# Kernel optimization log

Hardware: AMD Instinct MI355X
Metric: run time of the kernel (lower is better)

## Reference

```python
import jax, jax.numpy as jnp
import numpy as np

B, T, TKV, D, H = 4, 2048, 512, 1024, 16
HD = D // H  # 64
HIDDEN = ((int(D * 4 * 2 / 3) + 7) // 8) * 8  # 2736
EPS = 1e-6


def setup_inputs() -> dict:
    key = jax.random.key(0)
    ks = jax.random.split(key, 16)
    x = jax.random.normal(ks[0], (B, T, D), jnp.float32)
    memory = jax.random.normal(ks[1], (B, TKV, D), jnp.float32)
    # RoPE frequencies: (T, HD//2, 2) = (cos, sin)
    inv_freq = 1.0 / (10000.0 ** (jnp.arange(0, HD, 2, dtype=jnp.float32) / HD))
    angles = jnp.arange(T, dtype=jnp.float32)[:, None] * inv_freq[None, :]
    freqs_cis = jnp.stack([jnp.cos(angles), jnp.sin(angles)], axis=-1)
    # causal mask (T, T): 0 on/below diag, -inf above
    causal_mask = jnp.where(jnp.tril(jnp.ones((T, T), bool)), 0.0, -jnp.inf).astype(jnp.float32)
    s = 0.02
    w = lambda k, i, o: jax.random.normal(k, (i, o), jnp.float32) * s  # stored as (in, out)
    return {
        'x': x, 'memory': memory, 'freqs_cis': freqs_cis, 'causal_mask': causal_mask,
        'sa_wq': w(ks[2], D, D), 'sa_wk': w(ks[3], D, D), 'sa_wv': w(ks[4], D, D), 'sa_wo': w(ks[5], D, D),
        'ca_wq': w(ks[6], D, D), 'ca_wk': w(ks[7], D, D), 'ca_wv': w(ks[8], D, D), 'ca_wo': w(ks[9], D, D),
        'w1': w(ks[10], D, HIDDEN), 'w3': w(ks[11], D, HIDDEN), 'w2': w(ks[12], HIDDEN, D),
        'g_sa': jnp.ones((D,), jnp.float32), 'g_ca': jnp.ones((D,), jnp.float32), 'g_ffn': jnp.ones((D,), jnp.float32),
    }


def rmsnorm(x, g):
    return x * jax.lax.rsqrt(jnp.mean(x * x, axis=-1, keepdims=True) + EPS) * g


def apply_rope(t, f):
    # t: (B, H, T, HD); f: (T, HD//2, 2)
    tr = t.reshape(*t.shape[:-1], HD // 2, 2)
    a, b = tr[..., 0], tr[..., 1]
    cos, sin = f[None, None, :, :, 0], f[None, None, :, :, 1]
    out = jnp.stack([a * cos - b * sin, a * sin + b * cos], axis=-1)
    return out.reshape(t.shape)


def heads(x, w):
    # (B, S, D) @ (D, D) -> (B, H, S, HD)
    b, s, _ = x.shape
    return (x @ w).reshape(b, s, H, HD).transpose(0, 2, 1, 3)


def attention(xq, kv, wq, wk, wv, wo, freqs=None, mask=None):
    q, k, v = heads(xq, wq), heads(kv, wk), heads(kv, wv)
    if freqs is not None:
        q, k = apply_rope(q, freqs), apply_rope(k, freqs)
    attn = jnp.einsum('bhqd,bhkd->bhqk', q, k) * (HD ** -0.5)
    if mask is not None:
        attn = attn + mask
    attn = jax.nn.softmax(attn, axis=-1)
    out = jnp.einsum('bhqk,bhkd->bhqd', attn, v)
    out = out.transpose(0, 2, 1, 3).reshape(xq.shape[0], xq.shape[1], D)
    return out @ wo


def reference(x, memory, freqs_cis, causal_mask,
              sa_wq, sa_wk, sa_wv, sa_wo,
              ca_wq, ca_wk, ca_wv, ca_wo,
              w1, w2, w3, g_sa, g_ca, g_ffn):
    x = rmsnorm(x + attention(x, x, sa_wq, sa_wk, sa_wv, sa_wo, freqs=freqs_cis, mask=causal_mask), g_sa)
    x = rmsnorm(x + attention(x, memory, ca_wq, ca_wk, ca_wv, ca_wo), g_ca)
    ffn = (jax.nn.silu(x @ w1) * (x @ w3)) @ w2
    x = rmsnorm(x + ffn, g_ffn)
    return x
```

## Files before the change

kernel.cpp:

```cpp
#include <hip/hip_runtime.h>
#include <hip/hip_bf16.h>

typedef __attribute__((ext_vector_type(8))) short s16x8;
typedef __attribute__((ext_vector_type(4))) float f32x4;
typedef __attribute__((ext_vector_type(16))) float f32x16;
typedef unsigned short u16;
typedef unsigned int u32;
typedef unsigned long long u64;

#define MFMA(a,b,c) __builtin_amdgcn_mfma_f32_16x16x32_bf16(a,b,c,0,0,0)
#define MFMA32(a,b,c) __builtin_amdgcn_mfma_f32_32x32x16_bf16(a,b,c,0,0,0)

constexpr int B_ = 4, T_ = 2048, TKV_ = 512, D_ = 1024, H_ = 16, HD_ = 64;
constexpr int HID_ = 2736, HIDP_ = 2816;

__device__ __forceinline__ float bf2f(u16 x) {
    union { float f; u32 u; } c; c.u = ((u32)x) << 16; return c.f;
}
__device__ __forceinline__ u16 f2bf(float f) {
    union { float f; u32 u; } c; c.f = f;
    u32 r = c.u + 0x7fffu + ((c.u >> 16) & 1u);
    return (u16)(r >> 16);
}

__device__ __forceinline__ void gload16(const void* g, void* l) {
    __builtin_amdgcn_global_load_lds(
        (const __attribute__((address_space(1))) u32*)g,
        (__attribute__((address_space(3))) u32*)l, 16, 0, 0);
}

__global__ __launch_bounds__(256) void wt_cast(const float* __restrict__ W, u16* __restrict__ WT,
                                               int K, int N, int Kp, int Np) {
    __shared__ float t[32][33];
    int tid = threadIdx.x;
    int tx = tid & 31, ty = tid >> 5;
    int n0 = blockIdx.x * 32, k0 = blockIdx.y * 32;
#pragma unroll
    for (int i = 0; i < 4; ++i) {
        int kk = k0 + ty + i * 8, nn = n0 + tx;
        t[ty + i * 8][tx] = (kk < K && nn < N) ? W[(size_t)kk * N + nn] : 0.f;
    }
    __syncthreads();
#pragma unroll
    for (int i = 0; i < 4; ++i) {
        int nn = n0 + ty + i * 8, kk = k0 + tx;
        WT[(size_t)nn * Kp + kk] = f2bf(t[tx][ty + i * 8]);
    }
}

__global__ __launch_bounds__(256) void cast_bf16(const float* __restrict__ in, u16* __restrict__ out, int n4) {
    int i = blockIdx.x * 256 + threadIdx.x;
    if (i >= n4) return;
    float4 v = ((const float4*)in)[i];
    u64 pk = (u64)f2bf(v.x) | ((u64)f2bf(v.y) << 16) | ((u64)f2bf(v.z) << 32) | ((u64)f2bf(v.w) << 48);
    ((u64*)out)[i] = pk;
}

__global__ __launch_bounds__(256) void gemm_bf16(const u16* __restrict__ A, const u16* __restrict__ Bt,
                                                 void* __restrict__ C, const u16* __restrict__ mul,
                                                 int M, int N, int K, int mode, int nwg) {
    __shared__ __align__(16) u16 As[2][128 * 64];
    __shared__ __align__(16) u16 Bs[2][128 * 64];
    const int tid = threadIdx.x;
    const int lane = tid & 63, wid = tid >> 6;
    const int wr = wid >> 1, wc = wid & 1;
    const int li = lane & 15, g = lane >> 4;

    int bid = (int)blockIdx.x;
    bid = (bid & 7) * (nwg >> 3) + (bid >> 3);

    const int tn = N >> 7;
    const int m0 = (bid / tn) * 128, n0 = (bid % tn) * 128;

    const int rowst = tid >> 3;
    const int colb = (tid & 7) * 16;
    const char* ga = (const char*)A + ((size_t)(m0 + rowst) * K) * 2 + colb;
    const char* gb = (const char*)Bt + ((size_t)(n0 + rowst) * K) * 2 + colb;
    const size_t rstride = (size_t)32 * K * 2;

    f32x4 acc[4][4] = {};
    const int nt = K >> 6;

#pragma unroll
    for (int i = 0; i < 4; ++i) {
        gload16(ga + i * rstride, (char*)As[0] + i * 4096 + wid * 1024);
        gload16(gb + i * rstride, (char*)Bs[0] + i * 4096 + wid * 1024);
    }
    __syncthreads();

    int cur = 0;
    for (int t = 0; t < nt; ++t) {
        if (t + 1 < nt) {
            const char* gan = ga + (size_t)(t + 1) * 128;
            const char* gbn = gb + (size_t)(t + 1) * 128;
#pragma unroll
            for (int i = 0; i < 4; ++i) {
                gload16(gan + i * rstride, (char*)As[cur ^ 1] + i * 4096 + wid * 1024);
                gload16(gbn + i * rstride, (char*)Bs[cur ^ 1] + i * 4096 + wid * 1024);
            }
        }
#pragma unroll
        for (int kk = 0; kk < 2; ++kk) {
            s16x8 aF[4], bF[4];
#pragma unroll
            for (int m = 0; m < 4; ++m) aF[m] = *(const s16x8*)&As[cur][(wr * 64 + m * 16 + li) * 64 + kk * 32 + g * 8];
#pragma unroll
            for (int n = 0; n < 4; ++n) bF[n] = *(const s16x8*)&Bs[cur][(wc * 64 + n * 16 + li) * 64 + kk * 32 + g * 8];
#pragma unroll
            for (int m = 0; m < 4; ++m)
#pragma unroll
                for (int n = 0; n < 4; ++n)
                    acc[m][n] = MFMA(aF[m], bF[n], acc[m][n]);
        }
        __syncthreads();
        cur ^= 1;
    }

#pragma unroll
    for (int m = 0; m < 4; ++m)
#pragma unroll
        for (int n = 0; n < 4; ++n)
#pragma unroll
            for (int r = 0; r < 4; ++r) {
                size_t row = m0 + wr * 64 + m * 16 + g * 4 + r;
                size_t col = n0 + wc * 64 + n * 16 + li;
                size_t idx = row * N + col;
                float v = acc[m][n][r];
                if (mode == 0) {
                    ((float*)C)[idx] = v;
                } else if (mode == 1) {
                    ((u16*)C)[idx] = f2bf(v);
                } else if (mode == 2) {
                    float sg = 1.f / (1.f + __expf(-v));
                    ((u16*)C)[idx] = f2bf(v * sg);
                } else if (mode == 3) {
                    float h = bf2f(mul[idx]);
                    ((u16*)C)[idx] = f2bf(v * h);
                } else {
                    ((u16*)C)[idx] = f2bf(v * 0.125f);
                }
            }
}

__global__ __launch_bounds__(256) void rope_qk(u16* __restrict__ q, u16* __restrict__ k,
                                               const float* __restrict__ fr) {
    size_t idx = (size_t)blockIdx.x * 256 + threadIdx.x;
    int i = (int)(idx & 31);
    int h = (int)((idx >> 5) & 15);
    size_t bt = idx >> 9;
    int t = (int)(bt & (T_ - 1));
    float2 cs = ((const float2*)fr)[t * 32 + i];
    size_t off = bt * D_ + h * 64 + 2 * i;
    {
        u32* p = (u32*)(q + off);
        u32 w = *p;
        float a = bf2f((u16)(w & 0xffff)), b = bf2f((u16)(w >> 16));
        *p = (u32)f2bf((a * cs.x - b * cs.y) * 0.125f) | ((u32)f2bf((a * cs.y + b * cs.x) * 0.125f) << 16);
    }
    {
        u32* p = (u32*)(k + off);
        u32 w = *p;
        float a = bf2f((u16)(w & 0xffff)), b = bf2f((u16)(w >> 16));
        *p = (u32)f2bf(a * cs.x - b * cs.y) | ((u32)f2bf(a * cs.y + b * cs.x) << 16);
    }
}

__global__ __launch_bounds__(256) void vtrans(const u16* __restrict__ v, u16* __restrict__ vT, int Tk) {
    __shared__ u16 tile[32][34];
    int bh = blockIdx.x;
    int t0 = blockIdx.y * 32, d0 = blockIdx.z * 32;
    int b = bh >> 4, h = bh & 15;
    int tid = threadIdx.x;
    int tx = tid & 31, ty = tid >> 5;
#pragma unroll
    for (int i = 0; i < 4; ++i)
        tile[ty + i * 8][tx] = v[((size_t)b * Tk + t0 + ty + i * 8) * D_ + h * 64 + d0 + tx];
    __syncthreads();
#pragma unroll
    for (int i = 0; i < 4; ++i)
        vT[((size_t)bh * 64 + d0 + ty + i * 8) * Tk + t0 + tx] = tile[tx][ty + i * 8];
}

__device__ __forceinline__ void attn32(const u16* __restrict__ qh, const u16* __restrict__ kh,
                                       const u16* __restrict__ vh, u16* __restrict__ oh,
                                       int q0, int nkb, int Tk, int causal, int lq, int hi) {
    const u16* qb = qh + (size_t)(q0 + lq) * D_;
    s16x8 qf[4];
#pragma unroll
    for (int c = 0; c < 4; ++c) qf[c] = *(const s16x8*)&qb[c * 16 + hi * 8];

    f32x16 o0 = {}, o1 = {};
    float mr = -1e30f, lr = 0.f;

    for (int kb = 0; kb < nkb; ++kb) {
        const int ks = kb * 32;
        f32x16 s = {};
        const u16* kp = kh + (size_t)(ks + lq) * D_ + hi * 8;
#pragma unroll
        for (int c = 0; c < 4; ++c) {
            s16x8 kf = *(const s16x8*)&kp[c * 16];
            s = MFMA32(kf, qf[c], s);
        }
        if (causal && kb == nkb - 1) {
#pragma unroll
            for (int r = 0; r < 16; ++r) {
                int kl = (r & 3) + 8 * (r >> 2) + 4 * hi;
                if (kl > lq) s[r] = -1e30f;
            }
        }
        float bm = fmaxf(fmaxf(fmaxf(s[0], s[1]), fmaxf(s[2], s[3])),
                         fmaxf(fmaxf(s[4], s[5]), fmaxf(s[6], s[7])));
        float bm2 = fmaxf(fmaxf(fmaxf(s[8], s[9]), fmaxf(s[10], s[11])),
                          fmaxf(fmaxf(s[12], s[13]), fmaxf(s[14], s[15])));
        bm = fmaxf(bm, bm2);
        bm = fmaxf(bm, __shfl_xor(bm, 32));
        float mn = fmaxf(mr, bm);
        float sc = __expf(mr - mn);
        mr = mn;
        float p[16];
        float rs = 0.f;
#pragma unroll
        for (int r = 0; r < 16; ++r) { p[r] = __expf(s[r] - mn); rs += p[r]; }
        rs += __shfl_xor(rs, 32);
        lr = lr * sc + rs;
#pragma unroll
        for (int r = 0; r < 16; ++r) { o0[r] *= sc; o1[r] *= sc; }

        u32 pk[8];
#pragma unroll
        for (int i = 0; i < 8; ++i)
            pk[i] = (u32)f2bf(p[2 * i]) | ((u32)f2bf(p[2 * i + 1]) << 16);
        u32 e1 = __shfl_xor(hi ? pk[0] : pk[2], 32);
        u32 e2 = __shfl_xor(hi ? pk[1] : pk[3], 32);
        u32 e3 = __shfl_xor(hi ? pk[4] : pk[6], 32);
        u32 e4 = __shfl_xor(hi ? pk[5] : pk[7], 32);
        union { s16x8 v; u32 w[4]; } pf0, pf1;
        pf0.w[0] = hi ? e1 : pk[0];
        pf0.w[1] = hi ? e2 : pk[1];
        pf0.w[2] = hi ? pk[2] : e1;
        pf0.w[3] = hi ? pk[3] : e2;
        pf1.w[0] = hi ? e3 : pk[4];
        pf1.w[1] = hi ? e4 : pk[5];
        pf1.w[2] = hi ? pk[6] : e3;
        pf1.w[3] = hi ? pk[7] : e4;

        const u16* v0 = vh + (size_t)lq * Tk + ks + hi * 8;
        const u16* v1 = vh + (size_t)(32 + lq) * Tk + ks + hi * 8;
        o0 = MFMA32(*(const s16x8*)&v0[0],  pf0.v, o0);
        o0 = MFMA32(*(const s16x8*)&v0[16], pf1.v, o0);
        o1 = MFMA32(*(const s16x8*)&v1[0],  pf0.v, o1);
        o1 = MFMA32(*(const s16x8*)&v1[16], pf1.v, o1);
    }

    float inv = 1.f / lr;
    u16* ob = oh + (size_t)(q0 + lq) * D_;
#pragma unroll
    for (int r = 0; r < 16; ++r) {
        int hd = (r & 3) + 8 * (r >> 2) + 4 * hi;
        ob[hd] = f2bf(o0[r] * inv);
        ob[hd + 32] = f2bf(o1[r] * inv);
    }
}

__global__ __launch_bounds__(256) void attn_causal32(const u16* __restrict__ q, const u16* __restrict__ k,
                                                     const u16* __restrict__ vT, u16* __restrict__ o,
                                                     int Tq, int Tk) {
    const int lane = threadIdx.x & 63, wid = threadIdx.x >> 6;
    const int lq = lane & 31, hi = lane >> 5;
    const int ntile = Tq / 32;
    const int ppb = (ntile / 2) / 4;
    const int bh = blockIdx.x / ppb;
    const int p = (blockIdx.x % ppb) * 4 + wid;
    const int b = bh >> 4, h = bh & 15;

    const u16* qh = q + ((size_t)b * Tq) * D_ + h * 64;
    const u16* kh = k + ((size_t)b * Tk) * D_ + h * 64;
    const u16* vh = vT + ((size_t)bh * 64) * Tk;
    u16* oh = o + ((size_t)b * Tq) * D_ + h * 64;

    const int tA = p, tB = ntile - 1 - p;
    attn32(qh, kh, vh, oh, tA * 32, tA + 1, Tk, 1, lq, hi);
    attn32(qh, kh, vh, oh, tB * 32, tB + 1, Tk, 1, lq, hi);
}

__global__ __launch_bounds__(256) void attn_plain32(const u16* __restrict__ q, const u16* __restrict__ k,
                                                    const u16* __restrict__ vT, u16* __restrict__ o,
                                                    int Tq, int Tk) {
    const int lane = threadIdx.x & 63, wid = threadIdx.x >> 6;
    const int lq = lane & 31, hi = lane >> 5;
    const int tpb = (Tq / 32) / 4;
    const int bh = blockIdx.x / tpb;
    const int qt = (blockIdx.x % tpb) * 4 + wid;
    const int b = bh >> 4, h = bh & 15;

    const u16* qh = q + ((size_t)b * Tq) * D_ + h * 64;
    const u16* kh = k + ((size_t)b * Tk) * D_ + h * 64;
    const u16* vh = vT + ((size_t)bh * 64) * Tk;
    u16* oh = o + ((size_t)b * Tq) * D_ + h * 64;

    attn32(qh, kh, vh, oh, qt * 32, Tk / 32, Tk, 0, lq, hi);
}

__global__ __launch_bounds__(256) void addnorm(const float* __restrict__ xa, const float* __restrict__ xb,
                                               const float* __restrict__ gg, float* __restrict__ fo,
                                               u16* __restrict__ bo) {
    int row = blockIdx.x, tid = threadIdx.x;
    float4 a = ((const float4*)(xa + (size_t)row * D_))[tid];
    float4 b = ((const float4*)(xb + (size_t)row * D_))[tid];
    float vx = a.x + b.x, vy = a.y + b.y, vz = a.z + b.z, vw = a.w + b.w;
    float ss = vx * vx + vy * vy + vz * vz + vw * vw;
    ss += __shfl_xor(ss, 1);
    ss += __shfl_xor(ss, 2);
    ss += __shfl_xor(ss, 4);
    ss += __shfl_xor(ss, 8);
    ss += __shfl_xor(ss, 16);
    ss += __shfl_xor(ss, 32);
    __shared__ float red[4];
    int lane = tid & 63, wid = tid >> 6;
    if (lane == 0) red[wid] = ss;
    __syncthreads();
    float tot = red[0] + red[1] + red[2] + red[3];
    float s = rsqrtf(tot * (1.0f / D_) + 1e-6f);
    float4 gv = ((const float4*)gg)[tid];
    float yx = vx * s * gv.x, yy = vy * s * gv.y, yz = vz * s * gv.z, yw = vw * s * gv.w;
    if (fo) {
        float4 o4; o4.x = yx; o4.y = yy; o4.z = yz; o4.w = yw;
        ((float4*)(fo + (size_t)row * D_))[tid] = o4;
    }
    if (bo) {
        u64 pk = (u64)f2bf(yx) | ((u64)f2bf(yy) << 16) | ((u64)f2bf(yz) << 32) | ((u64)f2bf(yw) << 48);
        ((u64*)(bo + (size_t)row * D_))[tid] = pk;
    }
}

extern "C" void kernel_launch(void* const* d_in, const int* in_sizes, int n_in,
                              void* d_out, int out_size, void* d_ws, size_t ws_size,
                              hipStream_t stream) {
    const float* x    = (const float*)d_in[0];
    const float* mem  = (const float*)d_in[1];
    const float* fr   = (const float*)d_in[2];
    const float* wsaq = (const float*)d_in[4];
    const float* wsak = (const float*)d_in[5];
    const float* wsav = (const float*)d_in[6];
    const float* wsao = (const float*)d_in[7];
    const float* wcaq = (const float*)d_in[8];
    const float* wcak = (const float*)d_in[9];
    const float* wcav = (const float*)d_in[10];
    const float* wcao = (const float*)d_in[11];
    const float* w1   = (const float*)d_in[12];
    const float* w3   = (const float*)d_in[13];
    const float* w2   = (const float*)d_in[14];
    const float* g_sa = (const float*)d_in[15];
    const float* g_ca = (const float*)d_in[16];
    const float* g_ff = (const float*)d_in[17];
    float* outF = (float*)d_out;

    char* p = (char*)d_ws;
    auto alloc = [&](size_t bytes) { char* r = p; p += (bytes + 255) & ~(size_t)255; return r; };
    const size_t DD2 = (size_t)1024 * 1024 * 2;
    u16* saqT = (u16*)alloc(DD2);
    u16* sakT = (u16*)alloc(DD2);
    u16* savT = (u16*)alloc(DD2);
    u16* saoT = (u16*)alloc(DD2);
    u16* caqT = (u16*)alloc(DD2);
    u16* cakT = (u16*)alloc(DD2);
    u16* cavT = (u16*)alloc(DD2);
    u16* caoT = (u16*)alloc(DD2);
    u16* w1T  = (u16*)alloc((size_t)HIDP_ * 1024 * 2);
    u16* w3T  = (u16*)alloc((size_t)HIDP_ * 1024 * 2);
    u16* w2T  = (u16*)alloc((size_t)1024 * HIDP_ * 2);
    u16* Ab   = (u16*)alloc((size_t)8192 * 1024 * 2);
    u16* memb = (u16*)alloc((size_t)2048 * 1024 * 2);
    u16* qb   = (u16*)alloc((size_t)8192 * 1024 * 2);
    u16* kb   = (u16*)alloc((size_t)8192 * 1024 * 2);
    u16* vb   = (u16*)alloc((size_t)8192 * 1024 * 2);
    u16* vtb  = (u16*)alloc((size_t)8192 * 1024 * 2);
    u16* ob   = (u16*)alloc((size_t)8192 * 1024 * 2);
    float* Pf = (float*)alloc((size_t)8192 * 1024 * 4);
    float* Rf = (float*)alloc((size_t)8192 * 1024 * 4);
    u16* Hb   = (u16*)alloc((size_t)8192 * HIDP_ * 2);

    dim3 blk(256);

    wt_cast<<<dim3(32, 32), blk, 0, stream>>>(wsaq, saqT, 1024, 1024, 1024, 1024);
    wt_cast<<<dim3(32, 32), blk, 0, stream>>>(wsak, sakT, 1024, 1024, 1024, 1024);
    wt_cast<<<dim3(32, 32), blk, 0, stream>>>(wsav, savT, 1024, 1024, 1024, 1024);
    wt_cast<<<dim3(32, 32), blk, 0, stream>>>(wsao, saoT, 1024, 1024, 1024, 1024);
    wt_cast<<<dim3(32, 32), blk, 0, stream>>>(wcaq, caqT, 1024, 1024, 1024, 1024);
    wt_cast<<<dim3(32, 32), blk, 0, stream>>>(wcak, cakT, 1024, 1024, 1024, 1024);
    wt_cast<<<dim3(32, 32), blk, 0, stream>>>(wcav, cavT, 1024, 1024, 1024, 1024);
    wt_cast<<<dim3(32, 32), blk, 0, stream>>>(wcao, caoT, 1024, 1024, 1024, 1024);
    wt_cast<<<dim3(88, 32), blk, 0, stream>>>(w1, w1T, 1024, HID_, 1024, HIDP_);
    wt_cast<<<dim3(88, 32), blk, 0, stream>>>(w3, w3T, 1024, HID_, 1024, HIDP_);
    wt_cast<<<dim3(32, 88), blk, 0, stream>>>(w2, w2T, HID_, 1024, HIDP_, 1024);

    cast_bf16<<<8192, blk, 0, stream>>>(x, Ab, 2097152);
    cast_bf16<<<2048, blk, 0, stream>>>(mem, memb, 524288);

    gemm_bf16<<<512, blk, 0, stream>>>(Ab, saqT, qb, nullptr, 8192, 1024, 1024, 1, 512);
    gemm_bf16<<<512, blk, 0, stream>>>(Ab, sakT, kb, nullptr, 8192, 1024, 1024, 1, 512);
    gemm_bf16<<<512, blk, 0, stream>>>(Ab, savT, vb, nullptr, 8192, 1024, 1024, 1, 512);
    rope_qk<<<16384, blk, 0, stream>>>(qb, kb, fr);
    vtrans<<<dim3(64, 64, 2), blk, 0, stream>>>(vb, vtb, 2048);
    attn_causal32<<<512, blk, 0, stream>>>(qb, kb, vtb, ob, 2048, 2048);
    gemm_bf16<<<512, blk, 0, stream>>>(ob, saoT, Pf, nullptr, 8192, 1024, 1024, 0, 512);
    addnorm<<<8192, blk, 0, stream>>>(x, Pf, g_sa, Rf, Ab);

    gemm_bf16<<<512, blk, 0, stream>>>(Ab, caqT, qb, nullptr, 8192, 1024, 1024, 4, 512);
    gemm_bf16<<<128, blk, 0, stream>>>(memb, cakT, kb, nullptr, 2048, 1024, 1024, 1, 128);
    gemm_bf16<<<128, blk, 0, stream>>>(memb, cavT, vb, nullptr, 2048, 1024, 1024, 1, 128);
    vtrans<<<dim3(64, 16, 2), blk, 0, stream>>>(vb, vtb, 512);
    attn_plain32<<<1024, blk, 0, stream>>>(qb, kb, vtb, ob, 2048, 512);
    gemm_bf16<<<512, blk, 0, stream>>>(ob, caoT, Pf, nullptr, 8192, 1024, 1024, 0, 512);
    addnorm<<<8192, blk, 0, stream>>>(Rf, Pf, g_ca, Rf, Ab);

    gemm_bf16<<<64 * 22, blk, 0, stream>>>(Ab, w1T, Hb, nullptr, 8192, HIDP_, 1024, 2, 64 * 22);
    gemm_bf16<<<64 * 22, blk, 0, stream>>>(Ab, w3T, Hb, Hb, 8192, HIDP_, 1024, 3, 64 * 22);
    gemm_bf16<<<512, blk, 0, stream>>>(Hb, w2T, Pf, nullptr, 8192, 1024, HIDP_, 0, 512);
    addnorm<<<8192, blk, 0, stream>>>(Rf, Pf, g_ff, outF, nullptr);
}
```

Before: 945.1 us.

## Add 256x256-tile GEMM kernel and fuse QKV and cross-attention KV projections

```diff
diff --git a/kernel.cpp b/kernel.cpp
--- a/kernel.cpp
+++ b/kernel.cpp
@@ -54,6 +54,22 @@
     float4 v = ((const float4*)in)[i];
     u64 pk = (u64)f2bf(v.x) | ((u64)f2bf(v.y) << 16) | ((u64)f2bf(v.z) << 32) | ((u64)f2bf(v.w) << 48);
     ((u64*)out)[i] = pk;
+}
+
+__device__ __forceinline__ void gemm_store(void* C, const u16* mul, size_t idx, float v, int mode) {
+    if (mode == 0) {
+        ((float*)C)[idx] = v;
+    } else if (mode == 1) {
+        ((u16*)C)[idx] = f2bf(v);
+    } else if (mode == 2) {
+        float sg = 1.f / (1.f + __expf(-v));
+        ((u16*)C)[idx] = f2bf(v * sg);
+    } else if (mode == 3) {
+        float h = bf2f(mul[idx]);
+        ((u16*)C)[idx] = f2bf(v * h);
+    } else {
+        ((u16*)C)[idx] = f2bf(v * 0.125f);
+    }
 }
 
 __global__ __launch_bounds__(256) void gemm_bf16(const u16* __restrict__ A, const u16* __restrict__ Bt,
@@ -124,33 +140,91 @@
             for (int r = 0; r < 4; ++r) {
                 size_t row = m0 + wr * 64 + m * 16 + g * 4 + r;
                 size_t col = n0 + wc * 64 + n * 16 + li;
-                size_t idx = row * N + col;
-                float v = acc[m][n][r];
-                if (mode == 0) {
-                    ((float*)C)[idx] = v;
-                } else if (mode == 1) {
-                    ((u16*)C)[idx] = f2bf(v);
-                } else if (mode == 2) {
-                    float sg = 1.f / (1.f + __expf(-v));
-                    ((u16*)C)[idx] = f2bf(v * sg);
-                } else if (mode == 3) {
-                    float h = bf2f(mul[idx]);
-                    ((u16*)C)[idx] = f2bf(v * h);
-                } else {
-                    ((u16*)C)[idx] = f2bf(v * 0.125f);
-                }
+                gemm_store(C, mul, row * N + col, acc[m][n][r], mode);
+            }
+}
+
+__global__ __launch_bounds__(512) void gemm256(const u16* __restrict__ A, const u16* __restrict__ Bt,
+                                               void* __restrict__ C, const u16* __restrict__ mul,
+                                               int M, int N, int K, int mode, int nwg) {
+    __shared__ __align__(16) u16 As[2][256 * 64];
+    __shared__ __align__(16) u16 Bs[2][256 * 64];
+    const int tid = threadIdx.x;
+    const int lane = tid & 63, wid = tid >> 6;
+    const int wr = wid >> 2, wc = wid & 3;
+    const int li = lane & 15, g = lane >> 4;
+
+    int bid = (int)blockIdx.x;
+    bid = (bid & 7) * (nwg >> 3) + (bid >> 3);
+
+    const int tn = N >> 8;
+    const int m0 = (bid / tn) * 256, n0 = (bid % tn) * 256;
+
+    const int rowst = tid >> 3;
+    const int colb = (tid & 7) * 16;
+    const char* ga = (const char*)A + ((size_t)(m0 + rowst) * K) * 2 + colb;
+    const char* gb = (const char*)Bt + ((size_t)(n0 + rowst) * K) * 2 + colb;
+    const size_t rstride = (size_t)64 * K * 2;
+
+    f32x4 acc[8][4] = {};
+    const int nt = K >> 6;
+
+#pragma unroll
+    for (int i = 0; i < 4; ++i) {
+        gload16(ga + i * rstride, (char*)As[0] + i * 8192 + wid * 1024);
+        gload16(gb + i * rstride, (char*)Bs[0] + i * 8192 + wid * 1024);
+    }
+    __syncthreads();
+
+    int cur = 0;
+    for (int t = 0; t < nt; ++t) {
+        if (t + 1 < nt) {
+            const char* gan = ga + (size_t)(t + 1) * 128;
+            const char* gbn = gb + (size_t)(t + 1) * 128;
+#pragma unroll
+            for (int i = 0; i < 4; ++i) {
+                gload16(gan + i * rstride, (char*)As[cur ^ 1] + i * 8192 + wid * 1024);
+                gload16(gbn + i * rstride, (char*)Bs[cur ^ 1] + i * 8192 + wid * 1024);
+            }
+        }
+#pragma unroll
+        for (int kk = 0; kk < 2; ++kk) {
+            s16x8 bF[4];
+#pragma unroll
+            for (int n = 0; n < 4; ++n) bF[n] = *(const s16x8*)&Bs[cur][(wc * 64 + n * 16 + li) * 64 + kk * 32 + g * 8];
+#pragma unroll
+            for (int m = 0; m < 8; ++m) {
+                s16x8 aF = *(const s16x8*)&As[cur][(wr * 128 + m * 16 + li) * 64 + kk * 32 + g * 8];
+#pragma unroll
+                for (int n = 0; n < 4; ++n)
+                    acc[m][n] = MFMA(aF, bF[n], acc[m][n]);
+            }
+        }
+        __syncthreads();
+        cur ^= 1;
+    }
+
+#pragma unroll
+    for (int m = 0; m < 8; ++m)
+#pragma unroll
+        for (int n = 0; n < 4; ++n)
+#pragma unroll
+            for (int r = 0; r < 4; ++r) {
+                size_t row = m0 + wr * 128 + m * 16 + g * 4 + r;
+                size_t col = n0 + wc * 64 + n * 16 + li;
+                gemm_store(C, mul, row * N + col, acc[m][n][r], mode);
             }
 }
 
 __global__ __launch_bounds__(256) void rope_qk(u16* __restrict__ q, u16* __restrict__ k,
-                                               const float* __restrict__ fr) {
+                                               const float* __restrict__ fr, int S) {
     size_t idx = (size_t)blockIdx.x * 256 + threadIdx.x;
     int i = (int)(idx & 31);
     int h = (int)((idx >> 5) & 15);
     size_t bt = idx >> 9;
     int t = (int)(bt & (T_ - 1));
     float2 cs = ((const float2*)fr)[t * 32 + i];
-    size_t off = bt * D_ + h * 64 + 2 * i;
+    size_t off = bt * (size_t)S + h * 64 + 2 * i;
     {
         u32* p = (u32*)(q + off);
         u32 w = *p;
@@ -165,7 +239,8 @@
     }
 }
 
-__global__ __launch_bounds__(256) void vtrans(const u16* __restrict__ v, u16* __restrict__ vT, int Tk) {
+__global__ __launch_bounds__(256) void vtrans(const u16* __restrict__ v, u16* __restrict__ vT,
+                                              int Tk, int S) {
     __shared__ u16 tile[32][34];
     int bh = blockIdx.x;
     int t0 = blockIdx.y * 32, d0 = blockIdx.z * 32;
@@ -174,7 +249,7 @@
     int tx = tid & 31, ty = tid >> 5;
 #pragma unroll
     for (int i = 0; i < 4; ++i)
-        tile[ty + i * 8][tx] = v[((size_t)b * Tk + t0 + ty + i * 8) * D_ + h * 64 + d0 + tx];
+        tile[ty + i * 8][tx] = v[((size_t)b * Tk + t0 + ty + i * 8) * S + h * 64 + d0 + tx];
     __syncthreads();
 #pragma unroll
     for (int i = 0; i < 4; ++i)
@@ -183,8 +258,9 @@
 
 __device__ __forceinline__ void attn32(const u16* __restrict__ qh, const u16* __restrict__ kh,
                                        const u16* __restrict__ vh, u16* __restrict__ oh,
-                                       int q0, int nkb, int Tk, int causal, int lq, int hi) {
-    const u16* qb = qh + (size_t)(q0 + lq) * D_;
+                                       int q0, int nkb, int Tk, int causal, int lq, int hi,
+                                       int QS, int KS) {
+    const u16* qb = qh + (size_t)(q0 + lq) * QS;
     s16x8 qf[4];
 #pragma unroll
     for (int c = 0; c < 4; ++c) qf[c] = *(const s16x8*)&qb[c * 16 + hi * 8];
@@ -195,7 +271,7 @@
     for (int kb = 0; kb < nkb; ++kb) {
         const int ks = kb * 32;
         f32x16 s = {};
-        const u16* kp = kh + (size_t)(ks + lq) * D_ + hi * 8;
+        const u16* kp = kh + (size_t)(ks + lq) * KS + hi * 8;
 #pragma unroll
         for (int c = 0; c < 4; ++c) {
             s16x8 kf = *(const s16x8*)&kp[c * 16];
@@ -264,7 +340,7 @@
 
 __global__ __launch_bounds__(256) void attn_causal32(const u16* __restrict__ q, const u16* __restrict__ k,
                                                      const u16* __restrict__ vT, u16* __restrict__ o,
-                                                     int Tq, int Tk) {
+                                                     int Tq, int Tk, int QS, int KS) {
     const int lane = threadIdx.x & 63, wid = threadIdx.x >> 6;
     const int lq = lane & 31, hi = lane >> 5;
     const int ntile = Tq / 32;
@@ -273,19 +349,19 @@
     const int p = (blockIdx.x % ppb) * 4 + wid;
     const int b = bh >> 4, h = bh & 15;
 
-    const u16* qh = q + ((size_t)b * Tq) * D_ + h * 64;
-    const u16* kh = k + ((size_t)b * Tk) * D_ + h * 64;
+    const u16* qh = q + ((size_t)b * Tq) * QS + h * 64;
+    const u16* kh = k + ((size_t)b * Tk) * KS + h * 64;
     const u16* vh = vT + ((size_t)bh * 64) * Tk;
     u16* oh = o + ((size_t)b * Tq) * D_ + h * 64;
 
     const int tA = p, tB = ntile - 1 - p;
-    attn32(qh, kh, vh, oh, tA * 32, tA + 1, Tk, 1, lq, hi);
-    attn32(qh, kh, vh, oh, tB * 32, tB + 1, Tk, 1, lq, hi);
+    attn32(qh, kh, vh, oh, tA * 32, tA + 1, Tk, 1, lq, hi, QS, KS);
+    attn32(qh, kh, vh, oh, tB * 32, tB + 1, Tk, 1, lq, hi, QS, KS);
 }
 
 __global__ __launch_bounds__(256) void attn_plain32(const u16* __restrict__ q, const u16* __restrict__ k,
                                                     const u16* __restrict__ vT, u16* __restrict__ o,
-                                                    int Tq, int Tk) {
+                                                    int Tq, int Tk, int QS, int KS) {
     const int lane = threadIdx.x & 63, wid = threadIdx.x >> 6;
     const int lq = lane & 31, hi = lane >> 5;
     const int tpb = (Tq / 32) / 4;
@@ -293,12 +369,12 @@
     const int qt = (blockIdx.x % tpb) * 4 + wid;
     const int b = bh >> 4, h = bh & 15;
 
-    const u16* qh = q + ((size_t)b * Tq) * D_ + h * 64;
-    const u16* kh = k + ((size_t)b * Tk) * D_ + h * 64;
+    const u16* qh = q + ((size_t)b * Tq) * QS + h * 64;
+    const u16* kh = k + ((size_t)b * Tk) * KS + h * 64;
     const u16* vh = vT + ((size_t)bh * 64) * Tk;
     u16* oh = o + ((size_t)b * Tq) * D_ + h * 64;
 
-    attn32(qh, kh, vh, oh, qt * 32, Tk / 32, Tk, 0, lq, hi);
+    attn32(qh, kh, vh, oh, qt * 32, Tk / 32, Tk, 0, lq, hi, QS, KS);
 }
 
 __global__ __launch_bounds__(256) void addnorm(const float* __restrict__ xa, const float* __restrict__ xb,
@@ -358,37 +434,35 @@
     char* p = (char*)d_ws;
     auto alloc = [&](size_t bytes) { char* r = p; p += (bytes + 255) & ~(size_t)255; return r; };
     const size_t DD2 = (size_t)1024 * 1024 * 2;
-    u16* saqT = (u16*)alloc(DD2);
-    u16* sakT = (u16*)alloc(DD2);
-    u16* savT = (u16*)alloc(DD2);
-    u16* saoT = (u16*)alloc(DD2);
-    u16* caqT = (u16*)alloc(DD2);
-    u16* cakT = (u16*)alloc(DD2);
-    u16* cavT = (u16*)alloc(DD2);
-    u16* caoT = (u16*)alloc(DD2);
-    u16* w1T  = (u16*)alloc((size_t)HIDP_ * 1024 * 2);
-    u16* w3T  = (u16*)alloc((size_t)HIDP_ * 1024 * 2);
-    u16* w2T  = (u16*)alloc((size_t)1024 * HIDP_ * 2);
-    u16* Ab   = (u16*)alloc((size_t)8192 * 1024 * 2);
-    u16* memb = (u16*)alloc((size_t)2048 * 1024 * 2);
-    u16* qb   = (u16*)alloc((size_t)8192 * 1024 * 2);
-    u16* kb   = (u16*)alloc((size_t)8192 * 1024 * 2);
-    u16* vb   = (u16*)alloc((size_t)8192 * 1024 * 2);
+    u16* wqkvT = (u16*)alloc(3 * DD2);
+    u16* saoT  = (u16*)alloc(DD2);
+    u16* caqT  = (u16*)alloc(DD2);
+    u16* wkvT  = (u16*)alloc(2 * DD2);
+    u16* caoT  = (u16*)alloc(DD2);
+    u16* w1T   = (u16*)alloc((size_t)HIDP_ * 1024 * 2);
+    u16* w3T   = (u16*)alloc((size_t)HIDP_ * 1024 * 2);
+    u16* w2T   = (u16*)alloc((size_t)1024 * HIDP_ * 2);
+    u16* Ab    = (u16*)alloc((size_t)8192 * 1024 * 2);
+    u16* memb  = (u16*)alloc((size_t)2048 * 1024 * 2);
+    char* qkvRaw = alloc((size_t)8192 * 3072 * 2);
+    u16* qkvb = (u16*)qkvRaw;
+    u16* kvb  = (u16*)qkvRaw;
+    u16* caqb = (u16*)(qkvRaw + (size_t)25165824);
     u16* vtb  = (u16*)alloc((size_t)8192 * 1024 * 2);
     u16* ob   = (u16*)alloc((size_t)8192 * 1024 * 2);
     float* Pf = (float*)alloc((size_t)8192 * 1024 * 4);
     float* Rf = (float*)alloc((size_t)8192 * 1024 * 4);
     u16* Hb   = (u16*)alloc((size_t)8192 * HIDP_ * 2);
 
-    dim3 blk(256);
-
-    wt_cast<<<dim3(32, 32), blk, 0, stream>>>(wsaq, saqT, 1024, 1024, 1024, 1024);
-    wt_cast<<<dim3(32, 32), blk, 0, stream>>>(wsak, sakT, 1024, 1024, 1024, 1024);
-    wt_cast<<<dim3(32, 32), blk, 0, stream>>>(wsav, savT, 1024, 1024, 1024, 1024);
+    dim3 blk(256), blk5(512);
+
+    wt_cast<<<dim3(32, 32), blk, 0, stream>>>(wsaq, wqkvT,               1024, 1024, 1024, 1024);
+    wt_cast<<<dim3(32, 32), blk, 0, stream>>>(wsak, wqkvT + 1024 * 1024, 1024, 1024, 1024, 1024);
+    wt_cast<<<dim3(32, 32), blk, 0, stream>>>(wsav, wqkvT + 2048 * 1024, 1024, 1024, 1024, 1024);
     wt_cast<<<dim3(32, 32), blk, 0, stream>>>(wsao, saoT, 1024, 1024, 1024, 1024);
     wt_cast<<<dim3(32, 32), blk, 0, stream>>>(wcaq, caqT, 1024, 1024, 1024, 1024);
-    wt_cast<<<dim3(32, 32), blk, 0, stream>>>(wcak, cakT, 1024, 1024, 1024, 1024);
-    wt_cast<<<dim3(32, 32), blk, 0, stream>>>(wcav, cavT, 1024, 1024, 1024, 1024);
+    wt_cast<<<dim3(32, 32), blk, 0, stream>>>(wcak, wkvT,               1024, 1024, 1024, 1024);
+    wt_cast<<<dim3(32, 32), blk, 0, stream>>>(wcav, wkvT + 1024 * 1024, 1024, 1024, 1024, 1024);
     wt_cast<<<dim3(32, 32), blk, 0, stream>>>(wcao, caoT, 1024, 1024, 1024, 1024);
     wt_cast<<<dim3(88, 32), blk, 0, stream>>>(w1, w1T, 1024, HID_, 1024, HIDP_);
     wt_cast<<<dim3(88, 32), blk, 0, stream>>>(w3, w3T, 1024, HID_, 1024, HIDP_);
@@ -397,25 +471,22 @@
     cast_bf16<<<8192, blk, 0, stream>>>(x, Ab, 2097152);
     cast_bf16<<<2048, blk, 0, stream>>>(mem, memb, 524288);
 
-    gemm_bf16<<<512, blk, 0, stream>>>(Ab, saqT, qb, nullptr, 8192, 1024, 1024, 1, 512);
-    gemm_bf16<<<512, blk, 0, stream>>>(Ab, sakT, kb, nullptr, 8192, 1024, 1024, 1, 512);
-    gemm_bf16<<<512, blk, 0, stream>>>(Ab, savT, vb, nullptr, 8192, 1024, 1024, 1, 512);
-    rope_qk<<<16384, blk, 0, stream>>>(qb, kb, fr);
-    vtrans<<<dim3(64, 64, 2), blk, 0, stream>>>(vb, vtb, 2048);
-    attn_causal32<<<512, blk, 0, stream>>>(qb, kb, vtb, ob, 2048, 2048);
-    gemm_bf16<<<512, blk, 0, stream>>>(ob, saoT, Pf, nullptr, 8192, 1024, 1024, 0, 512);
+    gemm256<<<384, blk5, 0, stream>>>(Ab, wqkvT, qkvb, nullptr, 8192, 3072, 1024, 1, 384);
+    rope_qk<<<16384, blk, 0, stream>>>(qkvb, qkvb + 1024, fr, 3072);
+    vtrans<<<dim3(64, 64, 2), blk, 0, stream>>>(qkvb + 2048, vtb, 2048, 3072);
+    attn_causal32<<<512, blk, 0, stream>>>(qkvb, qkvb + 1024, vtb, ob, 2048, 2048, 3072, 3072);
+    gemm256<<<128, blk5, 0, stream>>>(ob, saoT, Pf, nullptr, 8192, 1024, 1024, 0, 128);
     addnorm<<<8192, blk, 0, stream>>>(x, Pf, g_sa, Rf, Ab);
 
-    gemm_bf16<<<512, blk, 0, stream>>>(Ab, caqT, qb, nullptr, 8192, 1024, 1024, 4, 512);
-    gemm_bf16<<<128, blk, 0, stream>>>(memb, cakT, kb, nullptr, 2048, 1024, 1024, 1, 128);
-    gemm_bf16<<<128, blk, 0, stream>>>(memb, cavT, vb, nullptr, 2048, 1024, 1024, 1, 128);
-    vtrans<<<dim3(64, 16, 2), blk, 0, stream>>>(vb, vtb, 512);
-    attn_plain32<<<1024, blk, 0, stream>>>(qb, kb, vtb, ob, 2048, 512);
-    gemm_bf16<<<512, blk, 0, stream>>>(ob, caoT, Pf, nullptr, 8192, 1024, 1024, 0, 512);
+    gemm256<<<128, blk5, 0, stream>>>(Ab, caqT, caqb, nullptr, 8192, 1024, 1024, 4, 128);
+    gemm_bf16<<<256, blk, 0, stream>>>(memb, wkvT, kvb, nullptr, 2048, 2048, 1024, 1, 256);
+    vtrans<<<dim3(64, 16, 2), blk, 0, stream>>>(kvb + 1024, vtb, 512, 2048);
+    attn_plain32<<<1024, blk, 0, stream>>>(caqb, kvb, vtb, ob, 2048, 512, 1024, 2048);
+    gemm256<<<128, blk5, 0, stream>>>(ob, caoT, Pf, nullptr, 8192, 1024, 1024, 0, 128);
     addnorm<<<8192, blk, 0, stream>>>(Rf, Pf, g_ca, Rf, Ab);
 
-    gemm_bf16<<<64 * 22, blk, 0, stream>>>(Ab, w1T, Hb, nullptr, 8192, HIDP_, 1024, 2, 64 * 22);
-    gemm_bf16<<<64 * 22, blk, 0, stream>>>(Ab, w3T, Hb, Hb, 8192, HIDP_, 1024, 3, 64 * 22);
-    gemm_bf16<<<512, blk, 0, stream>>>(Hb, w2T, Pf, nullptr, 8192, 1024, HIDP_, 0, 512);
+    gemm256<<<352, blk5, 0, stream>>>(Ab, w1T, Hb, nullptr, 8192, HIDP_, 1024, 2, 352);
+    gemm256<<<352, blk5, 0, stream>>>(Ab, w3T, Hb, Hb, 8192, HIDP_, 1024, 3, 352);
+    gemm256<<<128, blk5, 0, stream>>>(Hb, w2T, Pf, nullptr, 8192, 1024, HIDP_, 0, 128);
     addnorm<<<8192, blk, 0, stream>>>(Rf, Pf, g_ff, outF, nullptr);
 }
```

After: 1.173 ms. 1.24x slower.
